# Kernel tuning notes

Measured on AMD Instinct MI355X. Metric: run time of the kernel, lower is better.

## Reference

```python
import jax, jax.numpy as jnp
import numpy as np

N, S, E, H = 4, 2048, 1024, 16
D = E // H  # head dim = 64


def setup_inputs() -> dict:
    key = jax.random.key(0)
    ks = jax.random.split(key, 8)
    return {
        "values": jax.random.normal(ks[0], (N, S, E), dtype=jnp.float32),
        "keys": jax.random.normal(ks[1], (N, S, E), dtype=jnp.float32),
        "queries": jax.random.normal(ks[2], (N, S, E), dtype=jnp.float32),
        "mask": jnp.ones((N, 1, 1, S), dtype=jnp.int32),
        "Wv": jax.random.normal(ks[3], (D, D), dtype=jnp.float32) / np.sqrt(D),
        "Wk": jax.random.normal(ks[4], (D, D), dtype=jnp.float32) / np.sqrt(D),
        "Wq": jax.random.normal(ks[5], (D, D), dtype=jnp.float32) / np.sqrt(D),
        "W_out": jax.random.normal(ks[6], (E, E), dtype=jnp.float32) / np.sqrt(E),
        "b_out": jnp.zeros((E,), dtype=jnp.float32),
    }


def reference(values, keys, queries, mask, Wv, Wk, Wq, W_out, b_out):
    n, q_len = queries.shape[0], queries.shape[1]
    v = values.reshape(n, -1, H, D)
    k = keys.reshape(n, -1, H, D)
    q = queries.reshape(n, q_len, H, D)
    # per-head linear projections (torch Linear: x @ W.T), shared across heads
    v = jnp.einsum('nlhd,ed->nlhe', v, Wv)
    k = jnp.einsum('nlhd,ed->nlhe', k, Wk)
    q = jnp.einsum('nqhd,ed->nqhe', q, Wq)
    # full score tensor [n, h, q, k], faithful to the original einsum
    energy = jnp.einsum('nqhd,nkhd->nhqk', q, k)
    energy = jnp.where(mask == 0, jnp.float32(-1e20), energy)
    # NOTE: original scales by sqrt(embed_size), not sqrt(head_dim)
    attention = jax.nn.softmax(energy / jnp.sqrt(jnp.float32(E)), axis=3)
    out = jnp.einsum('nhql,nlhd->nqhd', attention, v).reshape(n, q_len, E)
    out = out @ W_out.T + b_out
    return out
```

## Files before the change

kernel.cpp:

```cpp
#include <hip/hip_runtime.h>
#include <stdint.h>

#define N_B 4
#define SEQ 2048
#define EMB 1024
#define NH  16
#define HD  64
#define NHT 64
#define BQ  128
#define BK  64

typedef __attribute__((ext_vector_type(8))) short bf16x8;
typedef __attribute__((ext_vector_type(4))) short bf16x4;
typedef __attribute__((ext_vector_type(4))) float f32x4;

__device__ __forceinline__ short f2bf(float x) {
  unsigned u = __float_as_uint(x);
  u += 0x7fffu + ((u >> 16) & 1u);
  return (short)(u >> 16);
}

#if __has_builtin(__builtin_amdgcn_cvt_pk_bf16_f32)
typedef __attribute__((ext_vector_type(2))) __bf16 bf16v2;
__device__ __forceinline__ unsigned pkbf(float a, float b) {
  bf16v2 r = __builtin_amdgcn_cvt_pk_bf16_f32(a, b);
  union { bf16v2 v; unsigned u; } c; c.v = r; return c.u;
}
#else
__device__ __forceinline__ unsigned pkbf(float a, float b) {
  return (unsigned)(unsigned short)f2bf(a) | ((unsigned)(unsigned short)f2bf(b) << 16);
}
#endif

__device__ __forceinline__ void glds16(const short* g, short* l) {
  __builtin_amdgcn_global_load_lds(
      (const __attribute__((address_space(1))) unsigned int*)g,
      (__attribute__((address_space(3))) unsigned int*)l, 16, 0, 0);
}

__device__ __forceinline__ int swz_src(int lane) {
  return (((lane & 7) ^ ((lane >> 3) & 7)) * 8) + ((lane >> 3) * 64);
}
__device__ __forceinline__ int swz_rd(int r, int k) {
  return r * 64 + ((k ^ (r & 7)) * 8);
}

__global__ __launch_bounds__(256) void projm_kernel(
    const float* __restrict__ Xq, const float* __restrict__ Xk, const float* __restrict__ Xv,
    const float* __restrict__ Wq, const float* __restrict__ Wk, const float* __restrict__ Wv,
    short* __restrict__ Qp, short* __restrict__ Kp, short* __restrict__ Vp,
    const float* __restrict__ Wo, short* __restrict__ Wb) {
  int tid = threadIdx.x;
  int z = blockIdx.z;
  if (z == 3) {
    int flat = blockIdx.x + blockIdx.y * 16;
    int idx = (flat * 256 + tid) * 4;
    f32x4 v = *(const f32x4*)(Wo + idx);
    uint2 u; u.x = pkbf(v.x, v.y); u.y = pkbf(v.z, v.w);
    *(uint2*)(Wb + idx) = u;
    return;
  }
  const float* X = (z == 0) ? Xq : (z == 1) ? Xk : Xv;
  const float* W = (z == 0) ? Wq : (z == 1) ? Wk : Wv;
  short* out = (z == 0) ? Qp : (z == 1) ? Kp : Vp;
  int transposed = (z == 2);

  __shared__ __attribute__((aligned(16))) short Xs[128 * 64];
  __shared__ __attribute__((aligned(16))) short Ws[64 * 64];
  int w = tid >> 6, lane = tid & 63;
  int quad = lane >> 4, l15 = lane & 15;
  int sb = blockIdx.x * 128;
  int nh = blockIdx.y;
  int n = nh >> 4, h = nh & 15;
  int r4 = tid >> 2, c0 = (tid & 3) * 16;
  int ch0 = c0 >> 3;
#pragma unroll
  for (int rr = 0; rr < 2; rr++) {
    int row = rr * 64 + r4;
    const float* gp = X + ((size_t)(n * SEQ + sb + row)) * EMB + h * HD + c0;
    f32x4 a = *(const f32x4*)gp, b = *(const f32x4*)(gp + 4);
    f32x4 c = *(const f32x4*)(gp + 8), d = *(const f32x4*)(gp + 12);
    uint4 u0, u1;
    u0.x = pkbf(a.x, a.y); u0.y = pkbf(a.z, a.w);
    u0.z = pkbf(b.x, b.y); u0.w = pkbf(b.z, b.w);
    u1.x = pkbf(c.x, c.y); u1.y = pkbf(c.z, c.w);
    u1.z = pkbf(d.x, d.y); u1.w = pkbf(d.z, d.w);
    *(uint4*)&Xs[row * 64 + ((ch0 ^ (row & 7)) * 8)] = u0;
    *(uint4*)&Xs[row * 64 + (((ch0 + 1) ^ (row & 7)) * 8)] = u1;
  }
  {
    int e = r4;
    const float* wp = W + e * HD + c0;
    f32x4 a = *(const f32x4*)wp, b = *(const f32x4*)(wp + 4);
    f32x4 c = *(const f32x4*)(wp + 8), d = *(const f32x4*)(wp + 12);
    uint4 u0, u1;
    u0.x = pkbf(a.x, a.y); u0.y = pkbf(a.z, a.w);
    u0.z = pkbf(b.x, b.y); u0.w = pkbf(b.z, b.w);
    u1.x = pkbf(c.x, c.y); u1.y = pkbf(c.z, c.w);
    u1.z = pkbf(d.x, d.y); u1.w = pkbf(d.z, d.w);
    *(uint4*)&Ws[e * 64 + ((ch0 ^ (e & 7)) * 8)] = u0;
    *(uint4*)&Ws[e * 64 + (((ch0 + 1) ^ (e & 7)) * 8)] = u1;
  }
  __syncthreads();
  f32x4 acc[2][4] = {};
#pragma unroll
  for (int ch = 0; ch < 2; ch++) {
    bf16x8 af[2], bfr[4];
#pragma unroll
    for (int mi = 0; mi < 2; mi++)
      af[mi] = *(const bf16x8*)&Xs[swz_rd(w * 32 + mi * 16 + l15, ch * 4 + quad)];
#pragma unroll
    for (int ni = 0; ni < 4; ni++)
      bfr[ni] = *(const bf16x8*)&Ws[swz_rd(ni * 16 + l15, ch * 4 + quad)];
#pragma unroll
    for (int mi = 0; mi < 2; mi++)
#pragma unroll
      for (int ni = 0; ni < 4; ni++)
        acc[mi][ni] = __builtin_amdgcn_mfma_f32_16x16x32_bf16(af[mi], bfr[ni], acc[mi][ni], 0, 0, 0);
  }
  if (!transposed) {
#pragma unroll
    for (int mi = 0; mi < 2; mi++)
#pragma unroll
      for (int ni = 0; ni < 4; ni++)
#pragma unroll
        for (int r = 0; r < 4; r++) {
          int s = sb + w * 32 + mi * 16 + quad * 4 + r;
          out[((size_t)nh * SEQ + s) * HD + ni * 16 + l15] = f2bf(acc[mi][ni][r]);
        }
  } else {
#pragma unroll
    for (int mi = 0; mi < 2; mi++)
#pragma unroll
      for (int ni = 0; ni < 4; ni++) {
        int e2 = ni * 16 + l15;
        int s0 = sb + w * 32 + mi * 16 + quad * 4;
        uint2 u;
        u.x = pkbf(acc[mi][ni][0], acc[mi][ni][1]);
        u.y = pkbf(acc[mi][ni][2], acc[mi][ni][3]);
        *(uint2*)(out + ((size_t)nh * HD + e2) * SEQ + s0) = u;
      }
  }
}

__global__ __launch_bounds__(256, 3) void attn_kernel(
    const short* __restrict__ Qg, const short* __restrict__ Kg,
    const short* __restrict__ Vg, const int* __restrict__ maskp,
    short* __restrict__ AO) {
  __shared__ __attribute__((aligned(16))) short KV[2][2][64 * 64];
  __shared__ __attribute__((aligned(16))) short QP[128 * 64];
  __shared__ int maskS[2][64];

  int tid = threadIdx.x;
  int w = tid >> 6, lane = tid & 63;
  int quad = lane >> 4, l15 = lane & 15;
  int nh = blockIdx.x;
  int qt0 = blockIdx.y * BQ;
  int n = nh >> 4, h = nh & 15;
  const float csc = 0.04508422f;
  int ssrc = swz_src(lane);
  int vrow = lane >> 3;
  int vcg = (((lane & 7) ^ ((lane >> 3) & 7)) * 8);

  const short* kb = Kg + (size_t)nh * SEQ * HD;
  const short* vb = Vg + (size_t)nh * HD * SEQ;

  const short* qbase = Qg + ((size_t)nh * SEQ + qt0) * HD;
#pragma unroll
  for (int i = 0; i < 4; i++) {
    int idx = (w * 4 + i) * 512;
    glds16(qbase + idx + ssrc, &QP[idx]);
  }
#pragma unroll
  for (int i = 0; i < 2; i++) {
    int idx = (w * 2 + i) * 512;
    glds16(kb + idx + ssrc, &KV[0][0][idx]);
    int d = (w * 2 + i) * 8 + vrow;
    glds16(vb + (size_t)d * SEQ + vcg, &KV[0][1][idx]);
  }
  if (tid < 64) maskS[0][tid] = maskp[n * SEQ + tid];
  __syncthreads();

  bf16x8 qf[2][2];
#pragma unroll
  for (int nt = 0; nt < 2; nt++)
#pragma unroll
    for (int ch = 0; ch < 2; ch++)
      qf[nt][ch] = *(const bf16x8*)&QP[swz_rd(w * 32 + nt * 16 + l15, ch * 4 + quad)];

  f32x4 Oacc[2][4] = {};
  float lsum[2] = {0.f, 0.f};
  short* psw = &QP[w * 2048];

  for (int kt = 0; kt < SEQ / BK; kt++) {
    int cur = kt & 1;
    const short* Kc = KV[cur][0];
    const short* Vc = KV[cur][1];
    if (kt + 1 < SEQ / BK) {
      int k0n = (kt + 1) * BK;
      short* Kn = KV[cur ^ 1][0];
      short* Vn = KV[cur ^ 1][1];
#pragma unroll
      for (int i = 0; i < 2; i++) {
        int idx = (w * 2 + i) * 512;
        glds16(kb + (size_t)k0n * HD + idx + ssrc, Kn + idx);
        int d = (w * 2 + i) * 8 + vrow;
        glds16(vb + (size_t)d * SEQ + k0n + vcg, Vn + idx);
      }
      if (tid < 64) maskS[cur ^ 1][tid] = maskp[n * SEQ + k0n + tid];
    }

    unsigned long long mb = __ballot(maskS[cur][lane] != 0);

    f32x4 st[4][2];
#pragma unroll
    for (int mt = 0; mt < 4; mt++) {
      bf16x8 kf0 = *(const bf16x8*)&Kc[swz_rd(mt * 16 + l15, quad)];
      bf16x8 kf1 = *(const bf16x8*)&Kc[swz_rd(mt * 16 + l15, 4 + quad)];
#pragma unroll
      for (int nt = 0; nt < 2; nt++) {
        f32x4 a = {0.f, 0.f, 0.f, 0.f};
        a = __builtin_amdgcn_mfma_f32_16x16x32_bf16(kf0, qf[nt][0], a, 0, 0, 0);
        a = __builtin_amdgcn_mfma_f32_16x16x32_bf16(kf1, qf[nt][1], a, 0, 0, 0);
        st[mt][nt] = a;
      }
    }
    if (mb != ~0ull) {
#pragma unroll
      for (int mt = 0; mt < 4; mt++)
#pragma unroll
        for (int r = 0; r < 4; r++) {
          int kk = mt * 16 + quad * 4 + r;
          if (!((mb >> kk) & 1)) { st[mt][0][r] = -1e20f; st[mt][1][r] = -1e20f; }
        }
    }
#pragma unroll
    for (int nt = 0; nt < 2; nt++)
#pragma unroll
      for (int mt = 0; mt < 4; mt++)
#pragma unroll
        for (int r = 0; r < 4; r++) {
          float p = __builtin_amdgcn_exp2f(st[mt][nt][r] * csc);
          st[mt][nt][r] = p;
          lsum[nt] += p;
        }
#pragma unroll
    for (int nt = 0; nt < 2; nt++) {
      int wrow = nt * 16 + l15;
#pragma unroll
      for (int mt = 0; mt < 4; mt++) {
        uint2 u;
        u.x = pkbf(st[mt][nt][0], st[mt][nt][1]);
        u.y = pkbf(st[mt][nt][2], st[mt][nt][3]);
        *(uint2*)&psw[wrow * 64 + (((mt * 2 + (quad >> 1)) ^ (wrow & 7)) * 8) + (quad & 1) * 4] = u;
      }
    }
    __builtin_amdgcn_wave_barrier();

#pragma unroll
    for (int ch = 0; ch < 2; ch++) {
      bf16x8 pf[2];
#pragma unroll
      for (int qt = 0; qt < 2; qt++)
        pf[qt] = *(const bf16x8*)&psw[swz_rd(qt * 16 + l15, ch * 4 + quad)];
#pragma unroll
      for (int dt = 0; dt < 4; dt++) {
        bf16x8 vf = *(const bf16x8*)&Vc[swz_rd(dt * 16 + l15, ch * 4 + quad)];
#pragma unroll
        for (int qt = 0; qt < 2; qt++)
          Oacc[qt][dt] = __builtin_amdgcn_mfma_f32_16x16x32_bf16(pf[qt], vf, Oacc[qt][dt], 0, 0, 0);
      }
    }
    __syncthreads();
  }
#pragma unroll
  for (int nt = 0; nt < 2; nt++) {
    lsum[nt] += __shfl_xor(lsum[nt], 16);
    lsum[nt] += __shfl_xor(lsum[nt], 32);
  }
#pragma unroll
  for (int qt = 0; qt < 2; qt++)
#pragma unroll
    for (int r = 0; r < 4; r++) {
      float lr = __shfl(lsum[qt], quad * 4 + r);
      float inv = 1.0f / lr;
      int qrow = qt0 + w * 32 + qt * 16 + quad * 4 + r;
      size_t rowb = ((size_t)n * SEQ + qrow) * EMB + h * HD;
#pragma unroll
      for (int dt = 0; dt < 4; dt++)
        AO[rowb + dt * 16 + l15] = f2bf(Oacc[qt][dt][r] * inv);
    }
}

__global__ __launch_bounds__(256, 2) void gemm_kernel(const short* __restrict__ A,
                                                      const short* __restrict__ B,
                                                      const float* __restrict__ bias,
                                                      float* __restrict__ C) {
  __shared__ __attribute__((aligned(16))) short As[2][128 * 64];
  __shared__ __attribute__((aligned(16))) short Bs[2][128 * 64];
  int tid = threadIdx.x;
  int w = tid >> 6, lane = tid & 63;
  int quad = lane >> 4, l15 = lane & 15;
  int m0 = blockIdx.x * 128, n0 = blockIdx.y * 128;
  int mw = (w & 1) * 64, nw = (w >> 1) * 64;
  int lrow = lane >> 3;
  int lcg = ((lane & 7) ^ ((lane >> 3) & 7)) * 8;
  f32x4 acc[4][4] = {};
#pragma unroll
  for (int i = 0; i < 4; i++) {
    int ii = w * 4 + i;
    int r = ii * 8 + lrow;
    glds16(A + (size_t)(m0 + r) * 1024 + lcg, &As[0][ii * 512]);
    glds16(B + (size_t)(n0 + r) * 1024 + lcg, &Bs[0][ii * 512]);
  }
  __syncthreads();
  for (int kt = 0; kt < 16; kt++) {
    int cur = kt & 1;
    if (kt < 15) {
      int k0n = (kt + 1) * 64;
#pragma unroll
      for (int i = 0; i < 4; i++) {
        int ii = w * 4 + i;
        int r = ii * 8 + lrow;
        glds16(A + (size_t)(m0 + r) * 1024 + k0n + lcg, &As[cur ^ 1][ii * 512]);
        glds16(B + (size_t)(n0 + r) * 1024 + k0n + lcg, &Bs[cur ^ 1][ii * 512]);
      }
    }
#pragma unroll
    for (int ch = 0; ch < 2; ch++) {
      bf16x8 af[4], bfr[4];
#pragma unroll
      for (int mi = 0; mi < 4; mi++)
        af[mi] = *(const bf16x8*)&As[cur][swz_rd(mw + mi * 16 + l15, ch * 4 + quad)];
#pragma unroll
      for (int ni = 0; ni < 4; ni++)
        bfr[ni] = *(const bf16x8*)&Bs[cur][swz_rd(nw + ni * 16 + l15, ch * 4 + quad)];
#pragma unroll
      for (int mi = 0; mi < 4; mi++)
#pragma unroll
        for (int ni = 0; ni < 4; ni++)
          acc[mi][ni] = __builtin_amdgcn_mfma_f32_16x16x32_bf16(af[mi], bfr[ni], acc[mi][ni], 0, 0, 0);
    }
    __syncthreads();
  }
#pragma unroll
  for (int ni = 0; ni < 4; ni++) {
    int col = n0 + nw + ni * 16 + l15;
    float bv = bias[col];
#pragma unroll
    for (int mi = 0; mi < 4; mi++) {
      int rb = m0 + mw + mi * 16 + quad * 4;
#pragma unroll
      for (int r = 0; r < 4; r++)
        C[(size_t)(rb + r) * 1024 + col] = acc[mi][ni][r] + bv;
    }
  }
}

extern "C" void kernel_launch(void* const* d_in, const int* in_sizes, int n_in,
                              void* d_out, int out_size, void* d_ws, size_t ws_size,
                              hipStream_t stream) {
  const float* values  = (const float*)d_in[0];
  const float* keys    = (const float*)d_in[1];
  const float* queries = (const float*)d_in[2];
  const int*   mask    = (const int*)d_in[3];
  const float* Wv = (const float*)d_in[4];
  const float* Wk = (const float*)d_in[5];
  const float* Wq = (const float*)d_in[6];
  const float* Wo = (const float*)d_in[7];
  const float* bo = (const float*)d_in[8];
  float* out = (float*)d_out;

  short* ws = (short*)d_ws;
  short* Qp = ws;
  short* Kp = Qp + (size_t)NHT * SEQ * HD;
  short* Vp = Kp + (size_t)NHT * SEQ * HD;
  short* AO = Vp + (size_t)NHT * SEQ * HD;
  short* Wb = AO + (size_t)N_B * SEQ * EMB;

  dim3 pg(SEQ / 128, NHT, 4);
  projm_kernel<<<pg, dim3(256), 0, stream>>>(queries, keys, values, Wq, Wk, Wv,
                                             Qp, Kp, Vp, Wo, Wb);
  dim3 ag(NHT, SEQ / BQ);
  attn_kernel<<<ag, dim3(256), 0, stream>>>(Qp, Kp, Vp, mask, AO);
  dim3 gg(8192 / 128, 1024 / 128);
  gemm_kernel<<<gg, dim3(256), 0, stream>>>(AO, Wb, bo, out);
}
```

Baseline: 285.9 us.

## Single-buffer K/V tiles for higher occupancy and compute row sums via MFMA

Replaces the double-buffered K/V shared tiles with single buffers loaded synchronously each iteration, halving LDS use so the launch bound can rise from 3 to 4 blocks per CU. Softmax row sums are now taken from an MFMA of the bf16 probabilities against a ones vector instead of per-lane adds and shuffles, and the exp is fused into the packing loop. The mask is prefetched into a register. This gives up the prefetch overlap of the next tile's global loads with compute and relies on extra resident waves to hide latency. Summing the rounded bf16 probabilities also changes normalization numerics slightly.

```diff
diff --git a/kernel.cpp b/kernel.cpp
--- a/kernel.cpp
+++ b/kernel.cpp
@@ -143,13 +143,13 @@
   }
 }
 
-__global__ __launch_bounds__(256, 3) void attn_kernel(
+__global__ __launch_bounds__(256, 4) void attn_kernel(
     const short* __restrict__ Qg, const short* __restrict__ Kg,
     const short* __restrict__ Vg, const int* __restrict__ maskp,
     short* __restrict__ AO) {
-  __shared__ __attribute__((aligned(16))) short KV[2][2][64 * 64];
+  __shared__ __attribute__((aligned(16))) short Ks[64 * 64];
+  __shared__ __attribute__((aligned(16))) short Vts[64 * 64];
   __shared__ __attribute__((aligned(16))) short QP[128 * 64];
-  __shared__ int maskS[2][64];
 
   int tid = threadIdx.x;
   int w = tid >> 6, lane = tid & 63;
@@ -161,6 +161,7 @@
   int ssrc = swz_src(lane);
   int vrow = lane >> 3;
   int vcg = (((lane & 7) ^ ((lane >> 3) & 7)) * 8);
+  const int NT = SEQ / BK;
 
   const short* kb = Kg + (size_t)nh * SEQ * HD;
   const short* vb = Vg + (size_t)nh * HD * SEQ;
@@ -171,16 +172,8 @@
     int idx = (w * 4 + i) * 512;
     glds16(qbase + idx + ssrc, &QP[idx]);
   }
-#pragma unroll
-  for (int i = 0; i < 2; i++) {
-    int idx = (w * 2 + i) * 512;
-    glds16(kb + idx + ssrc, &KV[0][0][idx]);
-    int d = (w * 2 + i) * 8 + vrow;
-    glds16(vb + (size_t)d * SEQ + vcg, &KV[0][1][idx]);
-  }
-  if (tid < 64) maskS[0][tid] = maskp[n * SEQ + tid];
+  int mcur = maskp[n * SEQ + lane];
   __syncthreads();
-
   bf16x8 qf[2][2];
 #pragma unroll
   for (int nt = 0; nt < 2; nt++)
@@ -188,35 +181,35 @@
     for (int ch = 0; ch < 2; ch++)
       qf[nt][ch] = *(const bf16x8*)&QP[swz_rd(w * 32 + nt * 16 + l15, ch * 4 + quad)];
 
+  bf16x8 vone;
+#pragma unroll
+  for (int j = 0; j < 8; j++) vone[j] = (short)0x3F80;
+
   f32x4 Oacc[2][4] = {};
-  float lsum[2] = {0.f, 0.f};
+  f32x4 lacc[2] = {};
   short* psw = &QP[w * 2048];
 
-  for (int kt = 0; kt < SEQ / BK; kt++) {
-    int cur = kt & 1;
-    const short* Kc = KV[cur][0];
-    const short* Vc = KV[cur][1];
-    if (kt + 1 < SEQ / BK) {
-      int k0n = (kt + 1) * BK;
-      short* Kn = KV[cur ^ 1][0];
-      short* Vn = KV[cur ^ 1][1];
-#pragma unroll
-      for (int i = 0; i < 2; i++) {
-        int idx = (w * 2 + i) * 512;
-        glds16(kb + (size_t)k0n * HD + idx + ssrc, Kn + idx);
-        int d = (w * 2 + i) * 8 + vrow;
-        glds16(vb + (size_t)d * SEQ + k0n + vcg, Vn + idx);
-      }
-      if (tid < 64) maskS[cur ^ 1][tid] = maskp[n * SEQ + k0n + tid];
-    }
-
-    unsigned long long mb = __ballot(maskS[cur][lane] != 0);
+  for (int kt = 0; kt < NT; kt++) {
+    int k0 = kt * BK;
+    __syncthreads();
+#pragma unroll
+    for (int i = 0; i < 2; i++) {
+      int idx = (w * 2 + i) * 512;
+      glds16(kb + (size_t)k0 * HD + idx + ssrc, &Ks[idx]);
+      int d = (w * 2 + i) * 8 + vrow;
+      glds16(vb + (size_t)d * SEQ + k0 + vcg, &Vts[idx]);
+    }
+    int knx = (kt + 1 < NT) ? kt + 1 : kt;
+    int mnxt = maskp[n * SEQ + knx * BK + lane];
+    __syncthreads();
+
+    unsigned long long mb = __ballot(mcur != 0);
 
     f32x4 st[4][2];
 #pragma unroll
     for (int mt = 0; mt < 4; mt++) {
-      bf16x8 kf0 = *(const bf16x8*)&Kc[swz_rd(mt * 16 + l15, quad)];
-      bf16x8 kf1 = *(const bf16x8*)&Kc[swz_rd(mt * 16 + l15, 4 + quad)];
+      bf16x8 kf0 = *(const bf16x8*)&Ks[swz_rd(mt * 16 + l15, quad)];
+      bf16x8 kf1 = *(const bf16x8*)&Ks[swz_rd(mt * 16 + l15, 4 + quad)];
 #pragma unroll
       for (int nt = 0; nt < 2; nt++) {
         f32x4 a = {0.f, 0.f, 0.f, 0.f};
@@ -235,23 +228,17 @@
         }
     }
 #pragma unroll
-    for (int nt = 0; nt < 2; nt++)
-#pragma unroll
-      for (int mt = 0; mt < 4; mt++)
-#pragma unroll
-        for (int r = 0; r < 4; r++) {
-          float p = __builtin_amdgcn_exp2f(st[mt][nt][r] * csc);
-          st[mt][nt][r] = p;
-          lsum[nt] += p;
-        }
-#pragma unroll
     for (int nt = 0; nt < 2; nt++) {
       int wrow = nt * 16 + l15;
 #pragma unroll
       for (int mt = 0; mt < 4; mt++) {
+        float p0 = __builtin_amdgcn_exp2f(st[mt][nt][0] * csc);
+        float p1 = __builtin_amdgcn_exp2f(st[mt][nt][1] * csc);
+        float p2 = __builtin_amdgcn_exp2f(st[mt][nt][2] * csc);
+        float p3 = __builtin_amdgcn_exp2f(st[mt][nt][3] * csc);
         uint2 u;
-        u.x = pkbf(st[mt][nt][0], st[mt][nt][1]);
-        u.y = pkbf(st[mt][nt][2], st[mt][nt][3]);
+        u.x = pkbf(p0, p1);
+        u.y = pkbf(p2, p3);
         *(uint2*)&psw[wrow * 64 + (((mt * 2 + (quad >> 1)) ^ (wrow & 7)) * 8) + (quad & 1) * 4] = u;
       }
     }
@@ -264,26 +251,23 @@
       for (int qt = 0; qt < 2; qt++)
         pf[qt] = *(const bf16x8*)&psw[swz_rd(qt * 16 + l15, ch * 4 + quad)];
 #pragma unroll
+      for (int qt = 0; qt < 2; qt++)
+        lacc[qt] = __builtin_amdgcn_mfma_f32_16x16x32_bf16(pf[qt], vone, lacc[qt], 0, 0, 0);
+#pragma unroll
       for (int dt = 0; dt < 4; dt++) {
-        bf16x8 vf = *(const bf16x8*)&Vc[swz_rd(dt * 16 + l15, ch * 4 + quad)];
+        bf16x8 vf = *(const bf16x8*)&Vts[swz_rd(dt * 16 + l15, ch * 4 + quad)];
 #pragma unroll
         for (int qt = 0; qt < 2; qt++)
           Oacc[qt][dt] = __builtin_amdgcn_mfma_f32_16x16x32_bf16(pf[qt], vf, Oacc[qt][dt], 0, 0, 0);
       }
     }
-    __syncthreads();
-  }
-#pragma unroll
-  for (int nt = 0; nt < 2; nt++) {
-    lsum[nt] += __shfl_xor(lsum[nt], 16);
-    lsum[nt] += __shfl_xor(lsum[nt], 32);
+    mcur = mnxt;
   }
 #pragma unroll
   for (int qt = 0; qt < 2; qt++)
 #pragma unroll
     for (int r = 0; r < 4; r++) {
-      float lr = __shfl(lsum[qt], quad * 4 + r);
-      float inv = 1.0f / lr;
+      float inv = 1.0f / lacc[qt][r];
       int qrow = qt0 + w * 32 + qt * 16 + quad * 4 + r;
       size_t rowb = ((size_t)n * SEQ + qrow) * EMB + h * HD;
 #pragma unroll
```

Measured after the change: 279.6 us. -2.2%, faster.
